# Kernel tuning notes

Measured on AMD Instinct MI355X. Metric: run time of the kernel, lower is better.

## Reference

```python
import jax, jax.numpy as jnp
import numpy as np

STEP = 0.1  # step_size from init
H = 2048    # ceil(dim/2)


def setup_inputs() -> dict:
    key = jax.random.key(0)
    k1, k2, k3 = jax.random.split(key, 3)
    B, h = 16384, H
    x = jax.random.normal(k1, (B, 2 * h), dtype=jnp.float32)
    # Xavier-uniform-like scale for [2h, h] linear weights
    scale = (6.0 / (h + 2 * h)) ** 0.5
    W0 = jax.random.normal(k2, (2 * h, h), dtype=jnp.float32) * scale
    W1 = jax.random.normal(k3, (2 * h, h), dtype=jnp.float32) * scale
    b0 = jnp.zeros((2 * h,), dtype=jnp.float32)
    b1 = jnp.zeros((2 * h,), dtype=jnp.float32)
    return {"x": x, "W0": W0, "b0": b0, "W1": W1, "b1": b1}


def reference(x, W0, b0, W1, b1):
    h = W0.shape[1]
    u_old = x[:, :h]          # [B, h]
    v_old = x[:, h:]          # [B, h]
    # stage 1: Linear(u) -> tanh -> W1^T matmul -> scaled residual add
    v_mid = jnp.tanh(u_old @ W1.T + b1)   # [B, 2h]
    v_sig = v_mid @ W1                     # [B, h]  (tied-weight transpose matmul)
    v_new = v_old + STEP * v_sig
    # stage 2: Linear(v_new) -> tanh -> W0^T matmul -> scaled residual sub
    u_mid = jnp.tanh(v_new @ W0.T + b0)   # [B, 2h]
    u_sig = u_mid @ W0                     # [B, h]
    u_new = u_old - STEP * u_sig
    return jnp.concatenate((u_new, v_new), axis=1)
```

## Files before the change

kernel.cpp:

```cpp
#include <hip/hip_runtime.h>
#include <hip/hip_bf16.h>
#include <stdint.h>


typedef __attribute__((ext_vector_type(8))) short short8;
typedef __attribute__((ext_vector_type(4))) float f32x4;

#define DEVINL __device__ __forceinline__

DEVINL ushort f2b(float f) {
  union { float f; uint32_t u; } v; v.f = f;
  uint32_t u = v.u;
  return (ushort)((u + 0x7fffu + ((u >> 16) & 1u)) >> 16);
}

DEVINL float fast_tanh(float x) {
  x = fminf(10.0f, fmaxf(-10.0f, x));
  float e = __expf(2.0f * x);
  return (e - 1.0f) * __builtin_amdgcn_rcpf(e + 1.0f);
}

DEVINL void gload16(const ushort* g, ushort* l) {
  __builtin_amdgcn_global_load_lds(
      (const __attribute__((address_space(1))) void*)g,
      (__attribute__((address_space(3))) void*)l, 16, 0, 0);
}

template<int MH, int NH>
DEVINL void mfma_quad(f32x4 (&acc)[8][4], const short8 (&a)[4][2],
                      const short8 (&b)[2][2]) {
#pragma unroll
  for (int ks = 0; ks < 2; ++ks)
#pragma unroll
    for (int mi = 0; mi < 4; ++mi)
#pragma unroll
      for (int ni = 0; ni < 2; ++ni)
        acc[MH * 4 + mi][NH * 2 + ni] = __builtin_amdgcn_mfma_f32_16x16x32_bf16(
            a[mi][ks], b[ni][ks], acc[MH * 4 + mi][NH * 2 + ni], 0, 0, 0);
}

template<int MODE, int SCHED>
DEVINL void gemm_body(const ushort* __restrict__ A, const ushort* __restrict__ Bt,
                      const float* __restrict__ bias, ushort* __restrict__ Tout,
                      const float* __restrict__ xres, float* __restrict__ outres,
                      ushort* __restrict__ vbout, float step, int M, int N, int K)
{
  constexpr int LDS_N = (SCHED == 3) ? 32768 : 65536;
  __shared__ __align__(16) ushort ldsU[LDS_N];

  const int tid  = threadIdx.x;
  const int wave = tid >> 6, lane = tid & 63;
  const int wr = wave >> 2, wc = wave & 3;
  const int lr = lane & 15, hi = lane >> 4;

  const int GX = gridDim.x;
  const int nwg = GX * gridDim.y;
  const int lin = blockIdx.y * GX + blockIdx.x;
  const int swz = (lin & 7) * (nwg >> 3) + (lin >> 3);
  const int by = swz / GX, bx = swz - by * GX;
  const int m0 = by * 256, n0 = bx * 256;

  const int kb_st = ((tid & 7) * 16) ^ (((tid >> 3) & 7) << 4);
  int offA[2][2], offB[2][2];
#pragma unroll
  for (int j = 0; j < 2; ++j) {
    const int rp = j * 64 + (tid >> 3);
#pragma unroll
    for (int h = 0; h < 2; ++h) {
      offA[h][j] = (m0 + (rp >> 6) * 128 + h * 64 + (rp & 63)) * K + (kb_st >> 1);
      offB[h][j] = (n0 + (rp >> 5) * 64 + h * 32 + (rp & 31)) * K + (kb_st >> 1);
    }
  }

#define STAGE_A(buf, half, t) do {                                             \
    gload16(A + (size_t)offA[half][0] + (size_t)(t) * 64,                      \
            ldsU + (buf) * 32768 + (half) * 8192 + tid * 8);                   \
    gload16(A + (size_t)offA[half][1] + (size_t)(t) * 64,                      \
            ldsU + (buf) * 32768 + (half) * 8192 + 4096 + tid * 8);            \
  } while (0)
#define STAGE_B(buf, half, t) do {                                             \
    gload16(Bt + (size_t)offB[half][0] + (size_t)(t) * 64,                     \
            ldsU + (buf) * 32768 + 16384 + (half) * 8192 + tid * 8);           \
    gload16(Bt + (size_t)offB[half][1] + (size_t)(t) * 64,                     \
            ldsU + (buf) * 32768 + 16384 + (half) * 8192 + 4096 + tid * 8);    \
  } while (0)

  const int xm = (lane & 7) << 4;
  const int kbr0 = (hi * 16) ^ xm;
  const int kbr1 = (64 + hi * 16) ^ xm;
  const int eA0 = (wr * 64 + lr) * 64 + (kbr0 >> 1);
  const int eA1 = (wr * 64 + lr) * 64 + (kbr1 >> 1);
  const int eB0 = (wc * 32 + lr) * 64 + (kbr0 >> 1);
  const int eB1 = (wc * 32 + lr) * 64 + (kbr1 >> 1);

#define LDSE(idx) (*(const short8*)&ldsU[idx])
#define READ_A8(dst, buf, half) do {                                           \
    dst[0][0] = LDSE((buf)*32768 + (half)*8192 +    0 + eA0);                  \
    dst[0][1] = LDSE((buf)*32768 + (half)*8192 +    0 + eA1);                  \
    dst[1][0] = LDSE((buf)*32768 + (half)*8192 + 1024 + eA0);                  \
    dst[1][1] = LDSE((buf)*32768 + (half)*8192 + 1024 + eA1);                  \
    dst[2][0] = LDSE((buf)*32768 + (half)*8192 + 2048 + eA0);                  \
    dst[2][1] = LDSE((buf)*32768 + (half)*8192 + 2048 + eA1);                  \
    dst[3][0] = LDSE((buf)*32768 + (half)*8192 + 3072 + eA0);                  \
    dst[3][1] = LDSE((buf)*32768 + (half)*8192 + 3072 + eA1);                  \
  } while (0)
#define READ_B4(dst, buf, half) do {                                           \
    dst[0][0] = LDSE((buf)*32768 + 16384 + (half)*8192 +    0 + eB0);          \
    dst[0][1] = LDSE((buf)*32768 + 16384 + (half)*8192 +    0 + eB1);          \
    dst[1][0] = LDSE((buf)*32768 + 16384 + (half)*8192 + 1024 + eB0);          \
    dst[1][1] = LDSE((buf)*32768 + 16384 + (half)*8192 + 1024 + eB1);          \
  } while (0)

  f32x4 acc[8][4] = {};
  short8 a0[4][2], a1[4][2], b0[2][2], b1[2][2];

#define VMW(n) asm volatile("s_waitcnt vmcnt(" #n ")" ::: "memory")
#define SCB __builtin_amdgcn_sched_barrier(0)
#define BAR __builtin_amdgcn_s_barrier()
#define LGK0 asm volatile("s_waitcnt lgkmcnt(0)" ::: "memory")

  const int NT = K >> 6;

  STAGE_A(0, 0, 0); STAGE_A(0, 1, 0); STAGE_B(0, 0, 0);
  STAGE_B(0, 1, 0);
#pragma unroll 1
  for (int t = 0; t < NT - 1; ++t) {
    VMW(2); BAR; SCB;
    READ_A8(a0, 0, 0); READ_B4(b0, 0, 0); READ_A8(a1, 0, 1);
    LGK0; SCB;
    BAR; SCB;
    STAGE_A(0, 0, t + 1); STAGE_A(0, 1, t + 1); STAGE_B(0, 0, t + 1);
    __builtin_amdgcn_s_setprio(1);
    mfma_quad<0, 0>(acc, a0, b0); mfma_quad<1, 0>(acc, a1, b0);
    __builtin_amdgcn_s_setprio(0);
    VMW(6); BAR; SCB;
    READ_B4(b1, 0, 1);
    LGK0; SCB;
    BAR; SCB;
    STAGE_B(0, 1, t + 1);
    __builtin_amdgcn_s_setprio(1);
    mfma_quad<0, 1>(acc, a0, b1); mfma_quad<1, 1>(acc, a1, b1);
    __builtin_amdgcn_s_setprio(0);
  }
  VMW(2); BAR; SCB;
  READ_A8(a0, 0, 0); READ_B4(b0, 0, 0); READ_A8(a1, 0, 1);
  LGK0; SCB;
  __builtin_amdgcn_s_setprio(1);
  mfma_quad<0, 0>(acc, a0, b0); mfma_quad<1, 0>(acc, a1, b0);
  __builtin_amdgcn_s_setprio(0);
  VMW(0); BAR; SCB;
  READ_B4(b1, 0, 1);
  LGK0; SCB;
  __builtin_amdgcn_s_setprio(1);
  mfma_quad<0, 1>(acc, a0, b1); mfma_quad<1, 1>(acc, a1, b1);
  __builtin_amdgcn_s_setprio(0);

  const int mrow0 = m0 + wr * 128 + hi * 4;
  const int ncol0 = n0 + wc * 64 + lr;
#pragma unroll
  for (int mi = 0; mi < 8; ++mi) {
#pragma unroll
    for (int ni = 0; ni < 4; ++ni) {
      const int col = ncol0 + ni * 16;
      if (MODE == 0) {
        const float bv = bias[col];
#pragma unroll
        for (int r = 0; r < 4; ++r) {
          const int row = mrow0 + mi * 16 + r;
          Tout[(size_t)row * N + col] = f2b(fast_tanh(acc[mi][ni][r] + bv));
        }
      } else {
#pragma unroll
        for (int r = 0; r < 4; ++r) {
          const int row = mrow0 + mi * 16 + r;
          const size_t oi = (size_t)row * 4096 + col;
          const float v = fmaf(step, acc[mi][ni][r], xres[oi]);
          outres[oi] = v;
          if (MODE == 1) vbout[(size_t)row * N + col] = f2b(v);
        }
      }
    }
  }
#undef STAGE_A
#undef STAGE_B
#undef LDSE
#undef READ_A8
#undef READ_B4
#undef VMW
#undef SCB
#undef BAR
#undef LGK0
}

__global__ __launch_bounds__(512, 2)
void gemm_t1(const ushort* A, const ushort* Bt, const float* bias,
             ushort* Tout, int M, int N, int K) {
  gemm_body<0, 3>(A, Bt, bias, Tout, nullptr, nullptr, nullptr, 0.f, M, N, K);
}
__global__ __launch_bounds__(512, 2)
void gemm_vnew(const ushort* A, const ushort* Bt, const float* xres,
               float* outres, ushort* vbout, float step, int M, int N, int K) {
  gemm_body<1, 3>(A, Bt, nullptr, nullptr, xres, outres, vbout, step, M, N, K);
}
__global__ __launch_bounds__(512, 2)
void gemm_t2(const ushort* A, const ushort* Bt, const float* bias,
             ushort* Tout, int M, int N, int K) {
  gemm_body<0, 3>(A, Bt, bias, Tout, nullptr, nullptr, nullptr, 0.f, M, N, K);
}
__global__ __launch_bounds__(512, 2)
void gemm_unew(const ushort* A, const ushort* Bt, const float* xres,
               float* outres, float step, int M, int N, int K) {
  gemm_body<2, 3>(A, Bt, nullptr, nullptr, xres, outres, nullptr, step, M, N, K);
}

__global__ void cast_strided_half(const float* __restrict__ x,
                                  ushort* __restrict__ dst)
{
  const int i = blockIdx.x * blockDim.x + threadIdx.x;
  const int row = i >> 9;
  const int c4  = (i & 511) * 4;
  const float4 v = *(const float4*)&x[(size_t)row * 4096 + c4];
  ushort4 o;
  o.x = f2b(v.x); o.y = f2b(v.y); o.z = f2b(v.z); o.w = f2b(v.w);
  *(ushort4*)&dst[(size_t)row * 2048 + c4] = o;
}

__global__ void pack_w(const float* __restrict__ W,
                       ushort* __restrict__ Wb, ushort* __restrict__ Wt)
{
  __shared__ float tile[32][33];
  const int bx = blockIdx.x * 32;
  const int by = blockIdx.y * 32;
  const int tx = threadIdx.x, ty = threadIdx.y;
#pragma unroll
  for (int j = ty; j < 32; j += 8) {
    const float v = W[(size_t)(by + j) * 2048 + bx + tx];
    tile[j][tx] = v;
    Wb[(size_t)(by + j) * 2048 + bx + tx] = f2b(v);
  }
  __syncthreads();
#pragma unroll
  for (int j = ty; j < 32; j += 8) {
    Wt[(size_t)(bx + j) * 4096 + by + tx] = f2b(tile[tx][j]);
  }
}

extern "C" void kernel_launch(void* const* d_in, const int* in_sizes, int n_in,
                              void* d_out, int out_size, void* d_ws, size_t ws_size,
                              hipStream_t stream)
{
  const float* x  = (const float*)d_in[0];
  const float* W0 = (const float*)d_in[1];
  const float* b0 = (const float*)d_in[2];
  const float* W1 = (const float*)d_in[3];
  const float* b1 = (const float*)d_in[4];
  float* out = (float*)d_out;

  const int Mrows = 16384, H2 = 4096, Hh = 2048;

  uint8_t* ws = (uint8_t*)d_ws;
  ushort* T   = (ushort*)ws;
  ushort* Ab  = (ushort*)(ws + (size_t)134217728);
  ushort* W0b = (ushort*)(ws + (size_t)134217728 + 67108864);
  ushort* W0t = W0b + 8388608;
  ushort* W1b = W0t + 8388608;
  ushort* W1t = W1b + 8388608;

  cast_strided_half<<<32768, 256, 0, stream>>>(x, Ab);
  dim3 pw_grid(64, 128), pw_blk(32, 8);
  pack_w<<<pw_grid, pw_blk, 0, stream>>>(W1, W1b, W1t);
  pack_w<<<pw_grid, pw_blk, 0, stream>>>(W0, W0b, W0t);

  dim3 blk(512);
  dim3 g1(H2 / 256, Mrows / 256);
  dim3 g2(Hh / 256, Mrows / 256);

  gemm_t1<<<g1, blk, 0, stream>>>(Ab, W1b, b1, T, Mrows, H2, Hh);
  gemm_vnew<<<g2, blk, 0, stream>>>(T, W1t, x + Hh, out + Hh, Ab, 0.1f,
                                    Mrows, Hh, H2);
  gemm_t2<<<g1, blk, 0, stream>>>(Ab, W0b, b0, T, Mrows, H2, Hh);
  gemm_unew<<<g2, blk, 0, stream>>>(T, W0t, x, out, -0.1f, Mrows, Hh, H2);
}
```

Measured before the change: 1.127 ms.

## Add double-buffered LDS pipeline schedule for first-stage GEMM kernels

Adds a new schedule that double-buffers the LDS tile: global loads for the next K-tile are issued into the other buffer before the current tile is read and consumed, with partial lgkmcnt waits so MFMAs start as soon as their fragments arrive. It replaces the single-buffer scheme, which needed extra barriers between reading and restaging. gemm_t1 and gemm_vnew now use it, while gemm_t2 and gemm_unew stay on the old schedule. The cost is twice the LDS per block (64K ushorts), which may limit occupancy to fewer blocks per CU than the launch bounds request. It also assumes an even number of K-tiles.

```diff
diff --git a/kernel.cpp b/kernel.cpp
--- a/kernel.cpp
+++ b/kernel.cpp
@@ -83,6 +83,10 @@
             ldsU + (buf) * 32768 + 16384 + (half) * 8192 + tid * 8);           \
     gload16(Bt + (size_t)offB[half][1] + (size_t)(t) * 64,                     \
             ldsU + (buf) * 32768 + 16384 + (half) * 8192 + 4096 + tid * 8);    \
+  } while (0)
+#define STAGE8(buf, t) do {                                                    \
+    STAGE_A(buf, 0, t); STAGE_A(buf, 1, t);                                    \
+    STAGE_B(buf, 0, t); STAGE_B(buf, 1, t);                                    \
   } while (0)
 
   const int xm = (lane & 7) << 4;
@@ -115,45 +119,74 @@
   short8 a0[4][2], a1[4][2], b0[2][2], b1[2][2];
 
 #define VMW(n) asm volatile("s_waitcnt vmcnt(" #n ")" ::: "memory")
+#define LGK(n) asm volatile("s_waitcnt lgkmcnt(" #n ")" ::: "memory")
 #define SCB __builtin_amdgcn_sched_barrier(0)
 #define BAR __builtin_amdgcn_s_barrier()
-#define LGK0 asm volatile("s_waitcnt lgkmcnt(0)" ::: "memory")
+#define PRIO1 __builtin_amdgcn_s_setprio(1)
+#define PRIO0 __builtin_amdgcn_s_setprio(0)
 
   const int NT = K >> 6;
 
-  STAGE_A(0, 0, 0); STAGE_A(0, 1, 0); STAGE_B(0, 0, 0);
-  STAGE_B(0, 1, 0);
+  if constexpr (SCHED == 5) {
+#define V5_TILE(buf, STG, VN)                                                  \
+    STG;                                                                       \
+    VMW(VN); SCB; BAR; SCB;                                                    \
+    READ_A8(a0, buf, 0); READ_B4(b0, buf, 0);                                  \
+    READ_A8(a1, buf, 1); READ_B4(b1, buf, 1);                                  \
+    LGK(12); SCB; PRIO1;                                                       \
+    mfma_quad<0, 0>(acc, a0, b0);                                              \
+    PRIO0; LGK(4); SCB; PRIO1;                                                 \
+    mfma_quad<1, 0>(acc, a1, b0);                                              \
+    PRIO0; LGK(0); SCB; PRIO1;                                                 \
+    mfma_quad<0, 1>(acc, a0, b1); mfma_quad<1, 1>(acc, a1, b1);                \
+    PRIO0; BAR;
+
+    STAGE8(0, 0);
+    const int NI = NT >> 1;
 #pragma unroll 1
-  for (int t = 0; t < NT - 1; ++t) {
+    for (int i = 0; i < NI - 1; ++i) {
+      const int t = 2 * i;
+      V5_TILE(0, STAGE8(1, t + 1), 8)
+      V5_TILE(1, STAGE8(0, t + 2), 8)
+    }
+    V5_TILE(0, STAGE8(1, NT - 1), 8)
+    V5_TILE(1, , 0)
+#undef V5_TILE
+  } else {
+    STAGE_A(0, 0, 0); STAGE_A(0, 1, 0); STAGE_B(0, 0, 0);
+    STAGE_B(0, 1, 0);
+#pragma unroll 1
+    for (int t = 0; t < NT - 1; ++t) {
+      VMW(2); BAR; SCB;
+      READ_A8(a0, 0, 0); READ_B4(b0, 0, 0); READ_A8(a1, 0, 1);
+      LGK(0); SCB;
+      BAR; SCB;
+      STAGE_A(0, 0, t + 1); STAGE_A(0, 1, t + 1); STAGE_B(0, 0, t + 1);
+      PRIO1;
+      mfma_quad<0, 0>(acc, a0, b0); mfma_quad<1, 0>(acc, a1, b0);
+      PRIO0;
+      VMW(6); BAR; SCB;
+      READ_B4(b1, 0, 1);
+      LGK(0); SCB;
+      BAR; SCB;
+      STAGE_B(0, 1, t + 1);
+      PRIO1;
+      mfma_quad<0, 1>(acc, a0, b1); mfma_quad<1, 1>(acc, a1, b1);
+      PRIO0;
+    }
     VMW(2); BAR; SCB;
     READ_A8(a0, 0, 0); READ_B4(b0, 0, 0); READ_A8(a1, 0, 1);
-    LGK0; SCB;
-    BAR; SCB;
-    STAGE_A(0, 0, t + 1); STAGE_A(0, 1, t + 1); STAGE_B(0, 0, t + 1);
-    __builtin_amdgcn_s_setprio(1);
+    LGK(0); SCB;
+    PRIO1;
     mfma_quad<0, 0>(acc, a0, b0); mfma_quad<1, 0>(acc, a1, b0);
-    __builtin_amdgcn_s_setprio(0);
-    VMW(6); BAR; SCB;
+    PRIO0;
+    VMW(0); BAR; SCB;
     READ_B4(b1, 0, 1);
-    LGK0; SCB;
-    BAR; SCB;
-    STAGE_B(0, 1, t + 1);
-    __builtin_amdgcn_s_setprio(1);
+    LGK(0); SCB;
+    PRIO1;
     mfma_quad<0, 1>(acc, a0, b1); mfma_quad<1, 1>(acc, a1, b1);
-    __builtin_amdgcn_s_setprio(0);
-  }
-  VMW(2); BAR; SCB;
-  READ_A8(a0, 0, 0); READ_B4(b0, 0, 0); READ_A8(a1, 0, 1);
-  LGK0; SCB;
-  __builtin_amdgcn_s_setprio(1);
-  mfma_quad<0, 0>(acc, a0, b0); mfma_quad<1, 0>(acc, a1, b0);
-  __builtin_amdgcn_s_setprio(0);
-  VMW(0); BAR; SCB;
-  READ_B4(b1, 0, 1);
-  LGK0; SCB;
-  __builtin_amdgcn_s_setprio(1);
-  mfma_quad<0, 1>(acc, a0, b1); mfma_quad<1, 1>(acc, a1, b1);
-  __builtin_amdgcn_s_setprio(0);
+    PRIO0;
+  }
 
   const int mrow0 = m0 + wr * 128 + hi * 4;
   const int ncol0 = n0 + wc * 64 + lr;
@@ -183,24 +216,27 @@
   }
 #undef STAGE_A
 #undef STAGE_B
+#undef STAGE8
 #undef LDSE
 #undef READ_A8
 #undef READ_B4
 #undef VMW
+#undef LGK
 #undef SCB
 #undef BAR
-#undef LGK0
+#undef PRIO1
+#undef PRIO0
 }
 
 __global__ __launch_bounds__(512, 2)
 void gemm_t1(const ushort* A, const ushort* Bt, const float* bias,
              ushort* Tout, int M, int N, int K) {
-  gemm_body<0, 3>(A, Bt, bias, Tout, nullptr, nullptr, nullptr, 0.f, M, N, K);
+  gemm_body<0, 5>(A, Bt, bias, Tout, nullptr, nullptr, nullptr, 0.f, M, N, K);
 }
 __global__ __launch_bounds__(512, 2)
 void gemm_vnew(const ushort* A, const ushort* Bt, const float* xres,
                float* outres, ushort* vbout, float step, int M, int N, int K) {
-  gemm_body<1, 3>(A, Bt, nullptr, nullptr, xres, outres, vbout, step, M, N, K);
+  gemm_body<1, 5>(A, Bt, nullptr, nullptr, xres, outres, vbout, step, M, N, K);
 }
 __global__ __launch_bounds__(512, 2)
 void gemm_t2(const ushort* A, const ushort* Bt, const float* bias,
```

After: 1.400 ms. 24.2% more time.
